# Optimization experiments

Measured on AMD Instinct MI355X. Metric: run time of the kernel, lower is better.

The kernel has to match this reference:

```python
import jax, jax.numpy as jnp
import numpy as np

N_NODES = 10000
N_EDGES = 160000
D_IN = 512
D_HID = 1024

def setup_inputs() -> dict:
    key = jax.random.key(0)
    ks = jax.random.split(key, 8)
    feat = jax.random.normal(ks[0], (N_NODES, D_IN), dtype=jnp.float32)
    W1 = jax.random.normal(ks[1], (D_IN, D_HID), dtype=jnp.float32) * (1.0 / np.sqrt(D_IN))
    b1 = jnp.zeros((D_HID,), dtype=jnp.float32)
    W2 = jax.random.normal(ks[2], (D_HID, D_IN), dtype=jnp.float32) * (1.0 / np.sqrt(D_HID))
    b2 = jnp.zeros((D_IN,), dtype=jnp.float32)
    eps = jnp.zeros((1,), dtype=jnp.float32)
    src = jax.random.randint(ks[3], (N_EDGES,), 0, N_NODES, dtype=jnp.int32)
    dst = jax.random.randint(ks[4], (N_EDGES,), 0, N_NODES, dtype=jnp.int32)
    return {"feat": feat, "W1": W1, "b1": b1, "W2": W2, "b2": b2,
            "eps": eps, "src": src, "dst": dst}

def reference(feat, W1, b1, W2, b2, eps, src, dst):
    # message passing: copy src feature along each edge, sum-reduce at dst
    msgs = feat[src]                                   # [E, D_IN] gather
    neigh = jax.ops.segment_sum(msgs, dst, num_segments=feat.shape[0])  # [N, D_IN]
    # GIN combine: (1 + eps) * self + sum(neighbors)
    rst = (1.0 + eps[0]) * feat + neigh
    # apply_func: 2-layer MLP with ReLU
    h = jnp.maximum(rst @ W1 + b1, 0.0)
    h = h @ W2 + b2
    # identity residual (in_dim == out_dim)
    return h + feat
```

## Files before the change

### kernel.cpp

```cpp
#include <hip/hip_runtime.h>

typedef unsigned short u16;
typedef unsigned int u32;
typedef __bf16 bf16x8 __attribute__((ext_vector_type(8)));
typedef float f32x4 __attribute__((ext_vector_type(4)));

#define N_NODES 10000
#define N_EDGES 160000
#define D_IN 512
#define D_HID 1024

#define AS1 __attribute__((address_space(1)))
#define AS3 __attribute__((address_space(3)))

__device__ __forceinline__ u16 f2bf(float f) {
    union { float f; u32 u; } v; v.f = f;
    return (u16)((v.u + 0x7fffu + ((v.u >> 16) & 1u)) >> 16);
}
__device__ __forceinline__ float b2f(u32 h) {
    union { u32 u; float f; } v; v.u = h << 16; return v.f;
}

__global__ __launch_bounds__(256) void prep_k(const int* __restrict__ dst,
                                              int* __restrict__ counts,
                                              const float* __restrict__ feat,
                                              u16* __restrict__ featb,
                                              const float* __restrict__ W1,
                                              u16* __restrict__ w1t,
                                              const float* __restrict__ W2,
                                              u16* __restrict__ w2t) {
    int b = blockIdx.x;
    int t = threadIdx.x;
    if (b < 625) {
        int e = b * 256 + t;
        if (e < N_EDGES) atomicAdd(&counts[dst[e]], 1);
        return;
    }
    if (b < 625 + 2500) {
        int i = ((b - 625) * 256 + t) * 8;
        float4 a = *(const float4*)(feat + i);
        float4 c = *(const float4*)(feat + i + 4);
        uint4 o;
        o.x = (u32)f2bf(a.x) | ((u32)f2bf(a.y) << 16);
        o.y = (u32)f2bf(a.z) | ((u32)f2bf(a.w) << 16);
        o.z = (u32)f2bf(c.x) | ((u32)f2bf(c.y) << 16);
        o.w = (u32)f2bf(c.z) | ((u32)f2bf(c.w) << 16);
        *(uint4*)(featb + i) = o;
        return;
    }
    __shared__ float tile[32][33];
    b -= 3125;
    const float* W; u16* WT; int K, N, nt;
    if (b < 512) { W = W1; WT = w1t; K = D_IN;  N = D_HID; nt = 32; }
    else         { b -= 512; W = W2; WT = w2t; K = D_HID; N = D_IN;  nt = 16; }
    int n0 = (b % nt) * 32, k0 = (b / nt) * 32;
    int tx = t & 31, ty = t >> 5;
#pragma unroll
    for (int i = 0; i < 32; i += 8)
        tile[ty + i][tx] = W[(size_t)(k0 + ty + i) * N + n0 + tx];
    __syncthreads();
#pragma unroll
    for (int i = 0; i < 32; i += 8)
        WT[(size_t)(n0 + ty + i) * K + k0 + tx] = f2bf(tile[tx][ty + i]);
}

__global__ __launch_bounds__(1024) void scan_k(const int* __restrict__ counts,
                                               int* __restrict__ offs,
                                               int* __restrict__ cursor) {
    __shared__ int wpre[16];
    int t = threadIdx.x, l = t & 63, w = t >> 6;
    int base = t * 10;
    int c[10];
    int lsum = 0;
#pragma unroll
    for (int i = 0; i < 10; i++) {
        int idx = base + i;
        c[i] = (idx < N_NODES) ? counts[idx] : 0;
        lsum += c[i];
    }
    int sc = lsum;
#pragma unroll
    for (int d = 1; d < 64; d <<= 1) {
        int v = __shfl_up(sc, d);
        if (l >= d) sc += v;
    }
    __shared__ int wsum[16];
    if (l == 63) wsum[w] = sc;
    __syncthreads();
    if (w == 0 && l < 16) {
        int v = wsum[l];
        int p = v;
#pragma unroll
        for (int d = 1; d < 16; d <<= 1) {
            int u = __shfl_up(p, d);
            if (l >= d) p += u;
        }
        wpre[l] = p - v;
    }
    __syncthreads();
    int run = wpre[w] + sc - lsum;
#pragma unroll
    for (int i = 0; i < 10; i++) {
        int idx = base + i;
        if (idx < N_NODES) { offs[idx] = run; cursor[idx] = run; run += c[i]; }
    }
    if (t == 1023) offs[N_NODES] = wpre[15] + sc;
}

__global__ void reorder_k(const int* __restrict__ src, const int* __restrict__ dst,
                          int* __restrict__ cursor, int* __restrict__ ssrc) {
    int e = blockIdx.x * 256 + threadIdx.x;
    if (e >= N_EDGES) return;
    int d = dst[e];
    int pos = atomicAdd(&cursor[d], 1);
    ssrc[pos] = src[e];
}

__global__ __launch_bounds__(128) void gather_k(const u16* __restrict__ featb,
                                                const float* __restrict__ eps,
                                                const int* __restrict__ offs,
                                                const int* __restrict__ ssrc,
                                                u16* __restrict__ out) {
    int n = (blockIdx.x * 128 + threadIdx.x) >> 6;
    int l = threadIdx.x & 63;
    if (n >= N_NODES) return;
    int beg = offs[n], end = offs[n + 1];
    float s = 1.0f + eps[0];
    uint4 sv = *(const uint4*)(featb + (size_t)n * D_IN + l * 8);
    float acc[8] = { s * b2f(sv.x & 0xffffu), s * b2f(sv.x >> 16),
                     s * b2f(sv.y & 0xffffu), s * b2f(sv.y >> 16),
                     s * b2f(sv.z & 0xffffu), s * b2f(sv.z >> 16),
                     s * b2f(sv.w & 0xffffu), s * b2f(sv.w >> 16) };
#define ACC4(v) \
        acc[0] += b2f(v.x & 0xffffu); acc[1] += b2f(v.x >> 16); \
        acc[2] += b2f(v.y & 0xffffu); acc[3] += b2f(v.y >> 16); \
        acc[4] += b2f(v.z & 0xffffu); acc[5] += b2f(v.z >> 16); \
        acc[6] += b2f(v.w & 0xffffu); acc[7] += b2f(v.w >> 16);
    int e = beg;
    for (; e + 8 <= end; e += 8) {
        uint4 v[8];
#pragma unroll
        for (int q = 0; q < 8; q++) {
            int iq = ssrc[e + q];
            v[q] = *(const uint4*)(featb + (size_t)iq * D_IN + l * 8);
        }
#pragma unroll
        for (int q = 0; q < 8; q++) { ACC4(v[q]) }
    }
    for (; e + 4 <= end; e += 4) {
        int i0 = ssrc[e], i1 = ssrc[e + 1], i2 = ssrc[e + 2], i3 = ssrc[e + 3];
        uint4 v0 = *(const uint4*)(featb + (size_t)i0 * D_IN + l * 8);
        uint4 v1 = *(const uint4*)(featb + (size_t)i1 * D_IN + l * 8);
        uint4 v2 = *(const uint4*)(featb + (size_t)i2 * D_IN + l * 8);
        uint4 v3 = *(const uint4*)(featb + (size_t)i3 * D_IN + l * 8);
        ACC4(v0) ACC4(v1) ACC4(v2) ACC4(v3)
    }
    for (; e < end; e++) {
        int i0 = ssrc[e];
        uint4 v0 = *(const uint4*)(featb + (size_t)i0 * D_IN + l * 8);
        ACC4(v0)
    }
#undef ACC4
    uint4 o;
    o.x = (u32)f2bf(acc[0]) | ((u32)f2bf(acc[1]) << 16);
    o.y = (u32)f2bf(acc[2]) | ((u32)f2bf(acc[3]) << 16);
    o.z = (u32)f2bf(acc[4]) | ((u32)f2bf(acc[5]) << 16);
    o.w = (u32)f2bf(acc[6]) | ((u32)f2bf(acc[7]) << 16);
    *(uint4*)(out + (size_t)n * D_IN + l * 8) = o;
}

template <int EPI, int K>
__global__ __launch_bounds__(64) void gemm_k(const u16* __restrict__ A,
                                             const u16* __restrict__ BT,
                                             const float* __restrict__ bias,
                                             const float* __restrict__ feat,
                                             void* __restrict__ Cout,
                                             int M, int N) {
    __shared__ __bf16 sA[3][64 * 32];
    __shared__ __bf16 sB[3][64 * 32];

    const int NX = gridDim.x;
    const int nwg = NX * gridDim.y;
    const int flat = blockIdx.y * NX + blockIdx.x;
    const int qq = nwg >> 3, rr8 = nwg & 7;
    const int xcd = flat & 7, idx = flat >> 3;
    const int L = (xcd < rr8 ? xcd * (qq + 1) : rr8 * (qq + 1) + (xcd - rr8) * qq) + idx;
    int row0 = (L / NX) * 64;
    if (row0 > M - 64) row0 = M - 64;
    const int col0 = (L % NX) * 64;

    const int l = threadIdx.x;
    const int lr = l & 15;
    const int lq = l >> 4;

    const int g8 = (((l & 3) ^ ((l >> 2) & 3)) * 8);
    const u16* bA = A  + (size_t)(row0 + (l >> 2)) * K + g8;
    const u16* bB = BT + (size_t)(col0 + (l >> 2)) * K + g8;
    const int fo = ((lq ^ (lr & 3)) * 8);

    f32x4 acc[4][4] = {};
    const int NT = K >> 5;

#define STAGE(buf, kt)                                                         \
    {                                                                          \
        const int ko_ = (kt) << 5;                                             \
        _Pragma("unroll")                                                      \
        for (int q_ = 0; q_ < 4; q_++) {                                       \
            __builtin_amdgcn_global_load_lds(                                  \
                (const AS1 void*)(bA + (size_t)q_ * 16 * K + ko_),             \
                (AS3 void*)(&sA[buf][q_ * 512]), 16, 0, 0);                    \
            __builtin_amdgcn_global_load_lds(                                  \
                (const AS1 void*)(bB + (size_t)q_ * 16 * K + ko_),             \
                (AS3 void*)(&sB[buf][q_ * 512]), 16, 0, 0);                    \
        }                                                                      \
    }

    STAGE(0, 0);
    STAGE(1, 1);

#pragma unroll
    for (int it = 0; it < NT; ++it) {
        const int cur = it % 3;
        if (it == NT - 1) {
            asm volatile("s_waitcnt vmcnt(0)" ::: "memory");
        } else {
            asm volatile("s_waitcnt vmcnt(8)" ::: "memory");
        }
        __builtin_amdgcn_sched_barrier(0);
        bf16x8 fa[4], fb[4];
#pragma unroll
        for (int i = 0; i < 4; i++)
            fa[i] = *(const bf16x8*)(&sA[cur][0] + (i * 16 + lr) * 32 + fo);
#pragma unroll
        for (int j = 0; j < 4; j++)
            fb[j] = *(const bf16x8*)(&sB[cur][0] + (j * 16 + lr) * 32 + fo);
        __builtin_amdgcn_sched_barrier(0);
        if (it + 2 < NT) STAGE((it + 2) % 3, it + 2);
        __builtin_amdgcn_sched_barrier(0);
#pragma unroll
        for (int i = 0; i < 4; i++)
#pragma unroll
            for (int j = 0; j < 4; j++)
                acc[i][j] = __builtin_amdgcn_mfma_f32_16x16x32_bf16(
                    fa[i], fb[j], acc[i][j], 0, 0, 0);
    }
#undef STAGE

#pragma unroll
    for (int i = 0; i < 4; i++) {
        int rowb = row0 + i * 16 + lq * 4;
#pragma unroll
        for (int j = 0; j < 4; j++) {
            int col = col0 + j * 16 + lr;
            float bv = bias[col];
#pragma unroll
            for (int r = 0; r < 4; r++) {
                int rr = rowb + r;
                float v = acc[i][j][r] + bv;
                if (EPI == 0) {
                    v = fmaxf(v, 0.0f);
                    ((u16*)Cout)[(size_t)rr * N + col] = f2bf(v);
                } else {
                    v += feat[(size_t)rr * N + col];
                    ((float*)Cout)[(size_t)rr * N + col] = v;
                }
            }
        }
    }
}

extern "C" void kernel_launch(void* const* d_in, const int* in_sizes, int n_in,
                              void* d_out, int out_size, void* d_ws, size_t ws_size,
                              hipStream_t stream) {
    const float* feat = (const float*)d_in[0];
    const float* W1   = (const float*)d_in[1];
    const float* b1   = (const float*)d_in[2];
    const float* W2   = (const float*)d_in[3];
    const float* b2   = (const float*)d_in[4];
    const float* eps  = (const float*)d_in[5];
    const int*   src  = (const int*)d_in[6];
    const int*   dst  = (const int*)d_in[7];
    float* out = (float*)d_out;

    char* ws = (char*)d_ws;
    u16* rst_b16 = (u16*)(ws);
    u16* h_b16   = (u16*)(ws + 10240000);
    u16* featb   = (u16*)(ws + 30720000);
    u16* w1t     = (u16*)(ws + 40960000);
    u16* w2t     = (u16*)(ws + 42008576);
    int* counts  = (int*)(ws + 43057152);
    int* offs    = (int*)(ws + 43097152);
    int* cursor  = (int*)(ws + 43137160);
    int* ssrc    = (int*)(ws + 43177160);

    hipMemsetAsync(counts, 0, N_NODES * sizeof(int), stream);
    prep_k<<<625 + 2500 + 1024, 256, 0, stream>>>(dst, counts, feat, featb,
                                                  W1, w1t, W2, w2t);
    scan_k<<<1, 1024, 0, stream>>>(counts, offs, cursor);
    reorder_k<<<(N_EDGES + 255) / 256, 256, 0, stream>>>(src, dst, cursor, ssrc);

    gather_k<<<(N_NODES + 1) / 2, 128, 0, stream>>>(featb, eps, offs, ssrc, rst_b16);

    const int MT = (N_NODES + 63) / 64;
    gemm_k<0, D_IN><<<dim3(D_HID / 64, MT), 64, 0, stream>>>(
        rst_b16, w1t, b1, nullptr, (void*)h_b16, N_NODES, D_HID);
    gemm_k<1, D_HID><<<dim3(D_IN / 64, MT), 64, 0, stream>>>(
        h_b16, w2t, b2, feat, (void*)out, N_NODES, D_IN);
}
```

Before: 183.9 us.

## Deepen GEMM LDS pipeline to four stages and double-buffer register fragments

The GEMM kernel moves from a 3-stage to a 4-stage LDS ring buffer, prefetching three k-tiles ahead. Register fragments are now double-buffered, so the LDS reads for the next tile are issued before the MFMAs of the current tile, overlapping LDS latency with matrix math. The cost is more LDS per workgroup and roughly twice the fragment registers, which can lower occupancy. The vmcnt wait counts are adjusted to the deeper prefetch.

```diff
diff --git a/kernel.cpp b/kernel.cpp
--- a/kernel.cpp
+++ b/kernel.cpp
@@ -176,8 +176,8 @@
                                              const float* __restrict__ feat,
                                              void* __restrict__ Cout,
                                              int M, int N) {
-    __shared__ __bf16 sA[3][64 * 32];
-    __shared__ __bf16 sB[3][64 * 32];
+    __shared__ __bf16 sA[4][64 * 32];
+    __shared__ __bf16 sB[4][64 * 32];
 
     const int NX = gridDim.x;
     const int nwg = NX * gridDim.y;
@@ -199,6 +199,7 @@
     const int fo = ((lq ^ (lr & 3)) * 8);
 
     f32x4 acc[4][4] = {};
+    bf16x8 fA[2][4], fB[2][4];
     const int NT = K >> 5;
 
 #define STAGE(buf, kt)                                                         \
@@ -215,35 +216,47 @@
         }                                                                      \
     }
 
+#define LOADFRAG(s, buf)                                                       \
+    {                                                                          \
+        _Pragma("unroll")                                                      \
+        for (int i_ = 0; i_ < 4; i_++)                                         \
+            fA[s][i_] = *(const bf16x8*)(&sA[buf][0] + (i_ * 16 + lr) * 32 + fo); \
+        _Pragma("unroll")                                                      \
+        for (int j_ = 0; j_ < 4; j_++)                                         \
+            fB[s][j_] = *(const bf16x8*)(&sB[buf][0] + (j_ * 16 + lr) * 32 + fo); \
+    }
+
     STAGE(0, 0);
     STAGE(1, 1);
+    STAGE(2, 2);
+    asm volatile("s_waitcnt vmcnt(16)" ::: "memory");
+    __builtin_amdgcn_sched_barrier(0);
+    LOADFRAG(0, 0);
 
 #pragma unroll
     for (int it = 0; it < NT; ++it) {
-        const int cur = it % 3;
-        if (it == NT - 1) {
-            asm volatile("s_waitcnt vmcnt(0)" ::: "memory");
-        } else {
-            asm volatile("s_waitcnt vmcnt(8)" ::: "memory");
+        if (it + 3 < NT) STAGE((it + 3) & 3, it + 3);
+        if (it < NT - 1) {
+            if (it <= NT - 4) {
+                asm volatile("s_waitcnt vmcnt(16)" ::: "memory");
+            } else if (it == NT - 3) {
+                asm volatile("s_waitcnt vmcnt(8)" ::: "memory");
+            } else {
+                asm volatile("s_waitcnt vmcnt(0)" ::: "memory");
+            }
+            __builtin_amdgcn_sched_barrier(0);
+            LOADFRAG((it + 1) & 1, (it + 1) & 3);
         }
         __builtin_amdgcn_sched_barrier(0);
-        bf16x8 fa[4], fb[4];
-#pragma unroll
-        for (int i = 0; i < 4; i++)
-            fa[i] = *(const bf16x8*)(&sA[cur][0] + (i * 16 + lr) * 32 + fo);
-#pragma unroll
-        for (int j = 0; j < 4; j++)
-            fb[j] = *(const bf16x8*)(&sB[cur][0] + (j * 16 + lr) * 32 + fo);
-        __builtin_amdgcn_sched_barrier(0);
-        if (it + 2 < NT) STAGE((it + 2) % 3, it + 2);
-        __builtin_amdgcn_sched_barrier(0);
+        const int s = it & 1;
 #pragma unroll
         for (int i = 0; i < 4; i++)
 #pragma unroll
             for (int j = 0; j < 4; j++)
                 acc[i][j] = __builtin_amdgcn_mfma_f32_16x16x32_bf16(
-                    fa[i], fb[j], acc[i][j], 0, 0, 0);
-    }
+                    fA[s][i], fB[s][j], acc[i][j], 0, 0, 0);
+    }
+#undef LOADFRAG
 #undef STAGE
 
 #pragma unroll
```

New measurement: 194.4 us. 5.7% more time.
